# Optimization experiments

Hardware: AMD Instinct MI355X
Metric: run time of the kernel (lower is better)

Reference implementation:

```python
import jax, jax.numpy as jnp
import numpy as np

B, T, C, H = 128, 256, 512, 512

def setup_inputs() -> dict:
    key = jax.random.key(0)
    k1, k2, k3, k4 = jax.random.split(key, 4)
    x = jax.random.normal(k1, (B, T, C), dtype=jnp.float32)
    # nn.Linear(n_embed, H_size, bias=False).weight has shape [H, C]; scaled init
    s = 1.0 / np.sqrt(C)
    Wq = jax.random.normal(k2, (H, C), dtype=jnp.float32) * s
    Wk = jax.random.normal(k3, (H, C), dtype=jnp.float32) * s
    Wv = jax.random.normal(k4, (H, C), dtype=jnp.float32) * s
    return {"x": x, "Wq": Wq, "Wk": Wk, "Wv": Wv}

def reference(x, Wq, Wk, Wv):
    # q,k,v: [B,T,H] = x @ W.T (torch Linear convention)
    q = jnp.einsum('btc,hc->bth', x, Wq)
    k = jnp.einsum('btc,hc->bth', x, Wk)
    v = jnp.einsum('btc,hc->bth', x, Wv)
    scale = k.shape[-1] ** -0.5
    score = jnp.einsum('bqh,bkh->bqk', q, k) * scale  # [B,T,T]
    # causal mask: position j attends to i only if i <= j
    i = jnp.arange(T)
    causal = i[None, :] <= i[:, None]  # [T,T] lower-triangular
    score = jnp.where(causal[None, :, :], score, -jnp.inf)
    attn = jax.nn.softmax(score, axis=-1)
    # dropout is identity in eval mode
    out = jnp.einsum('bqk,bkh->bqh', attn, v)  # [B,T,H]
    return out
```

## Files before the change

### kernel.cpp

```cpp
#include <hip/hip_runtime.h>

#define B_ 128
#define T_ 256
#define C_ 512
#define H_ 512
#define CSCALE 0.063763824f

typedef _Float16 f16x8 __attribute__((ext_vector_type(8)));
typedef _Float16 f16x4 __attribute__((ext_vector_type(4)));
typedef float    f32x4 __attribute__((ext_vector_type(4)));

__device__ __forceinline__ void gld16(const void* gsrc, void* ldst) {
  __builtin_amdgcn_global_load_lds(
      (__attribute__((address_space(1))) void*)gsrc,
      (__attribute__((address_space(3))) void*)ldst, 16, 0, 0);
}

__global__ __launch_bounds__(256) void cvt_kernel(
    const float4* __restrict__ x, const float4* __restrict__ wq,
    const float4* __restrict__ wk, const float4* __restrict__ wv,
    f16x4* __restrict__ dst) {
  const int NX = (B_ * T_ * C_) / 4;
  const int NW = (H_ * C_) / 4;
  const int total = NX + 3 * NW;
  int gid = blockIdx.x * 256 + threadIdx.x;
  int gsz = gridDim.x * 256;
  for (int i = gid; i < total; i += gsz) {
    float4 f;
    if (i < NX)            f = x[i];
    else if (i < NX + NW)  f = wq[i - NX];
    else if (i < NX + 2*NW) f = wk[i - NX - NW];
    else                   f = wv[i - NX - 2*NW];
    f16x4 u = {(_Float16)f.x, (_Float16)f.y, (_Float16)f.z, (_Float16)f.w};
    dst[i] = u;
  }
}

__global__ __launch_bounds__(256) void proj_kernel(
    const _Float16* __restrict__ xh, const _Float16* __restrict__ wh,
    _Float16* __restrict__ qh, _Float16* __restrict__ kh,
    _Float16* __restrict__ vth) {
  __shared__ _Float16 As[128 * 32];
  __shared__ _Float16 Bs[128 * 32];

  const int tid  = threadIdx.x;
  const int lane = tid & 63;
  const int wave = tid >> 6;
  const int lr = lane & 15, lk = lane >> 4;
  const int m0 = blockIdx.x * 128;
  const int n0 = blockIdx.y * 128;
  const int z  = blockIdx.z;
  const _Float16* wz = wh + z * (H_ * C_);

  const int wm = (wave >> 1) * 64;
  const int wn = (wave & 1) * 64;

  f32x4 acc[4][4];
#pragma unroll
  for (int i = 0; i < 4; ++i)
#pragma unroll
    for (int j = 0; j < 4; ++j) acc[i][j] = {0.f, 0.f, 0.f, 0.f};

  const int srow = tid >> 2, scol = (tid & 3) * 8;
  const _Float16* aSrc = xh + (m0 + srow) * C_ + scol;
  const _Float16* bSrc = wz + (n0 + srow) * C_ + scol;

  for (int k0 = 0; k0 < C_; k0 += 32) {
    __syncthreads();
#pragma unroll
    for (int i = 0; i < 2; ++i) {
      gld16((const void*)(aSrc + i * 64 * C_ + k0), (void*)&As[i * 2048 + wave * 512]);
      gld16((const void*)(bSrc + i * 64 * C_ + k0), (void*)&Bs[i * 2048 + wave * 512]);
    }
    __syncthreads();

    f16x8 a[4], b[4];
#pragma unroll
    for (int mi = 0; mi < 4; ++mi)
      a[mi] = *(const f16x8*)&As[(wm + mi * 16 + lr) * 32 + lk * 8];
#pragma unroll
    for (int ni = 0; ni < 4; ++ni)
      b[ni] = *(const f16x8*)&Bs[(wn + ni * 16 + lr) * 32 + lk * 8];
#pragma unroll
    for (int mi = 0; mi < 4; ++mi)
#pragma unroll
      for (int ni = 0; ni < 4; ++ni)
        acc[mi][ni] = __builtin_amdgcn_mfma_f32_16x16x32_f16(a[mi], b[ni], acc[mi][ni], 0, 0, 0);
  }

  if (z < 2) {
    _Float16* out = (z == 0) ? qh : kh;
#pragma unroll
    for (int mi = 0; mi < 4; ++mi) {
      int mbase = m0 + wm + mi * 16 + lk * 4;
#pragma unroll
      for (int ni = 0; ni < 4; ++ni) {
        int n = n0 + wn + ni * 16 + lr;
#pragma unroll
        for (int r = 0; r < 4; ++r)
          out[(mbase + r) * H_ + n] = (_Float16)acc[mi][ni][r];
      }
    }
  } else {
#pragma unroll
    for (int mi = 0; mi < 4; ++mi) {
      int mbase = m0 + wm + mi * 16 + lk * 4;
      int bb = mbase >> 8, tt = mbase & 255;
#pragma unroll
      for (int ni = 0; ni < 4; ++ni) {
        int n = n0 + wn + ni * 16 + lr;
        f16x4 u = {(_Float16)acc[mi][ni][0], (_Float16)acc[mi][ni][1],
                   (_Float16)acc[mi][ni][2], (_Float16)acc[mi][ni][3]};
        *(f16x4*)&vth[bb * (H_ * T_) + n * T_ + tt] = u;
      }
    }
  }
}

__global__ __launch_bounds__(128) void attn_kernel(
    const _Float16* __restrict__ qh, const _Float16* __restrict__ kh,
    const _Float16* __restrict__ vth, float* __restrict__ dout) {
  __shared__ _Float16 Ps[2 * 16 * 40];

  const int tid  = threadIdx.x;
  const int lane = tid & 63;
  const int wq   = tid >> 6;
  const int lr = lane & 15, lk = lane >> 4;
  const int flat = blockIdx.x;
  const int xcd  = flat & 7;
  const int rest = flat >> 3;
  const int p    = rest & 7;
  const int g    = rest >> 3;
  const int b    = xcd + (g << 3);
  const int qw = wq ? (15 - p) : p;
  const int q0 = qw * 16;
  const int nkv = (qw >> 1) + 1;

  f16x8 qf[16];
  const _Float16* qrow = qh + ((size_t)b * T_ + q0 + lr) * H_;
#pragma unroll
  for (int f = 0; f < 16; ++f) qf[f] = *(const f16x8*)&qrow[f * 32 + lk * 8];

  f32x4 o[32];
#pragma unroll
  for (int i = 0; i < 32; ++i) o[i] = {0.f, 0.f, 0.f, 0.f};
  float m[4], l[4];
#pragma unroll
  for (int r = 0; r < 4; ++r) { m[r] = -1e30f; l[r] = 0.f; }

  const _Float16* kbase = kh + (size_t)b * T_ * H_;
  const _Float16* vbase = vth + (size_t)b * H_ * T_;
  _Float16* Pw = &Ps[wq * 640];

  for (int kvt = 0; kvt < nkv; ++kvt) {
    const int kv0 = kvt * 32;

    f32x4 s0 = {0.f, 0.f, 0.f, 0.f}, s1 = {0.f, 0.f, 0.f, 0.f};
    f32x4 t0 = {0.f, 0.f, 0.f, 0.f}, t1 = {0.f, 0.f, 0.f, 0.f};
    const _Float16* krow0 = kbase + (size_t)(kv0 + lr) * H_ + lk * 8;
    const _Float16* krow1 = krow0 + 16 * H_;
#pragma unroll
    for (int ks = 0; ks < 16; ks += 2) {
      f16x8 b0 = *(const f16x8*)&krow0[ks * 32];
      f16x8 b1 = *(const f16x8*)&krow1[ks * 32];
      f16x8 c0 = *(const f16x8*)&krow0[ks * 32 + 32];
      f16x8 c1 = *(const f16x8*)&krow1[ks * 32 + 32];
      s0 = __builtin_amdgcn_mfma_f32_16x16x32_f16(qf[ks], b0, s0, 0, 0, 0);
      s1 = __builtin_amdgcn_mfma_f32_16x16x32_f16(qf[ks], b1, s1, 0, 0, 0);
      t0 = __builtin_amdgcn_mfma_f32_16x16x32_f16(qf[ks + 1], c0, t0, 0, 0, 0);
      t1 = __builtin_amdgcn_mfma_f32_16x16x32_f16(qf[ks + 1], c1, t1, 0, 0, 0);
    }
    s0 = s0 + t0;
    s1 = s1 + t1;

    float p0[4], p1[4], rm[4];
    const int rowb = q0 + lk * 4;
#pragma unroll
    for (int r = 0; r < 4; ++r) {
      float v0 = (kv0 + lr      > rowb + r) ? -1e30f : s0[r];
      float v1 = (kv0 + 16 + lr > rowb + r) ? -1e30f : s1[r];
      s0[r] = v0; s1[r] = v1;
      rm[r] = fmaxf(v0, v1);
    }
#pragma unroll
    for (int off = 1; off < 16; off <<= 1)
#pragma unroll
      for (int r = 0; r < 4; ++r) rm[r] = fmaxf(rm[r], __shfl_xor(rm[r], off, 64));

    bool need = false;
#pragma unroll
    for (int r = 0; r < 4; ++r) need = need || (rm[r] > m[r] + 64.f);
    if (__any(need)) {
#pragma unroll
      for (int r = 0; r < 4; ++r) {
        float mn = fmaxf(m[r], rm[r]);
        float al = __builtin_amdgcn_exp2f((m[r] - mn) * CSCALE);
        m[r] = mn; l[r] *= al;
#pragma unroll
        for (int hf = 0; hf < 32; ++hf) o[hf][r] *= al;
      }
    }

    float rs[4];
#pragma unroll
    for (int r = 0; r < 4; ++r) {
      p0[r] = __builtin_amdgcn_exp2f((s0[r] - m[r]) * CSCALE);
      p1[r] = __builtin_amdgcn_exp2f((s1[r] - m[r]) * CSCALE);
      rs[r] = p0[r] + p1[r];
    }
#pragma unroll
    for (int off = 1; off < 16; off <<= 1)
#pragma unroll
      for (int r = 0; r < 4; ++r) rs[r] += __shfl_xor(rs[r], off, 64);
#pragma unroll
    for (int r = 0; r < 4; ++r) l[r] += rs[r];

#pragma unroll
    for (int r = 0; r < 4; ++r) {
      Pw[(lk * 4 + r) * 40 + lr]      = (_Float16)p0[r];
      Pw[(lk * 4 + r) * 40 + 16 + lr] = (_Float16)p1[r];
    }
    f16x8 pa = *(const f16x8*)&Pw[lr * 40 + lk * 8];

    const _Float16* vcol = vbase + (size_t)lr * T_ + kv0 + lk * 8;
#pragma unroll
    for (int hf = 0; hf < 32; ++hf) {
      f16x8 vb = *(const f16x8*)&vcol[(size_t)hf * 16 * T_];
      o[hf] = __builtin_amdgcn_mfma_f32_16x16x32_f16(pa, vb, o[hf], 0, 0, 0);
    }
  }

  float linv[4];
#pragma unroll
  for (int r = 0; r < 4; ++r) linv[r] = 1.0f / l[r];
  float* orow = dout + ((size_t)b * T_ + q0 + lk * 4) * H_;
#pragma unroll
  for (int hf = 0; hf < 32; ++hf)
#pragma unroll
    for (int r = 0; r < 4; ++r)
      orow[(size_t)r * H_ + hf * 16 + lr] = o[hf][r] * linv[r];
}

extern "C" void kernel_launch(void* const* d_in, const int* in_sizes, int n_in,
                              void* d_out, int out_size, void* d_ws, size_t ws_size,
                              hipStream_t stream) {
  const size_t NXE = (size_t)B_ * T_ * C_;
  const size_t NWE = (size_t)3 * H_ * C_;
  const size_t NQE = (size_t)B_ * T_ * H_;
  const size_t need = (NXE + NWE + 3 * NQE) * sizeof(_Float16);
  if (ws_size < need) return;

  const float* x  = (const float*)d_in[0];
  const float* wq = (const float*)d_in[1];
  const float* wk = (const float*)d_in[2];
  const float* wv = (const float*)d_in[3];

  _Float16* xh  = (_Float16*)d_ws;
  _Float16* wh  = xh + NXE;
  _Float16* qh  = wh + NWE;
  _Float16* kh  = qh + NQE;
  _Float16* vth = kh + NQE;

  cvt_kernel<<<2048, 256, 0, stream>>>((const float4*)x, (const float4*)wq,
                                       (const float4*)wk, (const float4*)wv,
                                       (f16x4*)xh);
  proj_kernel<<<dim3(256, 4, 3), dim3(256), 0, stream>>>(xh, wh, qh, kh, vth);
  attn_kernel<<<1024, 128, 0, stream>>>(qh, kh, vth, (float*)d_out);
}
```

Measured before the change: 202.2 us.

## Split attention head dimension across four waves with LDS score reduction

Each attention block now handles a single 16-row query tile, and its four waves each own a 128-wide slice of the head dimension. Every wave computes partial QK^T scores for its slice, and the partials are summed through shared memory with two barriers per KV tile. Per-thread registers for Q fragments and O accumulators drop to a quarter of what they were, which allows higher occupancy and twice as many blocks. In exchange, the softmax and exp work is duplicated across the four waves and the per-tile barriers add synchronisation cost.

```diff
diff --git a/kernel.cpp b/kernel.cpp
--- a/kernel.cpp
+++ b/kernel.cpp
@@ -117,10 +117,11 @@
   }
 }
 
-__global__ __launch_bounds__(128) void attn_kernel(
+__global__ __launch_bounds__(256, 4) void attn_kernel(
     const _Float16* __restrict__ qh, const _Float16* __restrict__ kh,
     const _Float16* __restrict__ vth, float* __restrict__ dout) {
-  __shared__ _Float16 Ps[2 * 16 * 40];
+  __shared__ f32x4 Sx[2][4][64];
+  __shared__ _Float16 Ps[4 * 16 * 40];
 
   const int tid  = threadIdx.x;
   const int lane = tid & 63;
@@ -129,49 +130,55 @@
   const int flat = blockIdx.x;
   const int xcd  = flat & 7;
   const int rest = flat >> 3;
-  const int p    = rest & 7;
-  const int g    = rest >> 3;
+  const int qw   = 15 - (rest & 15);
+  const int g    = rest >> 4;
   const int b    = xcd + (g << 3);
-  const int qw = wq ? (15 - p) : p;
   const int q0 = qw * 16;
   const int nkv = (qw >> 1) + 1;
-
-  f16x8 qf[16];
-  const _Float16* qrow = qh + ((size_t)b * T_ + q0 + lr) * H_;
-#pragma unroll
-  for (int f = 0; f < 16; ++f) qf[f] = *(const f16x8*)&qrow[f * 32 + lk * 8];
-
-  f32x4 o[32];
-#pragma unroll
-  for (int i = 0; i < 32; ++i) o[i] = {0.f, 0.f, 0.f, 0.f};
+  const int hbase = wq * 128;
+
+  f16x8 qf[4];
+  const _Float16* qrow = qh + ((size_t)b * T_ + q0 + lr) * H_ + hbase;
+#pragma unroll
+  for (int f = 0; f < 4; ++f) qf[f] = *(const f16x8*)&qrow[f * 32 + lk * 8];
+
+  f32x4 o[8];
+#pragma unroll
+  for (int i = 0; i < 8; ++i) o[i] = {0.f, 0.f, 0.f, 0.f};
   float m[4], l[4];
 #pragma unroll
   for (int r = 0; r < 4; ++r) { m[r] = -1e30f; l[r] = 0.f; }
 
-  const _Float16* kbase = kh + (size_t)b * T_ * H_;
-  const _Float16* vbase = vth + (size_t)b * H_ * T_;
+  const _Float16* kbase = kh + (size_t)b * T_ * H_ + hbase;
+  const _Float16* vbase = vth + ((size_t)b * H_ + hbase) * T_;
   _Float16* Pw = &Ps[wq * 640];
 
   for (int kvt = 0; kvt < nkv; ++kvt) {
     const int kv0 = kvt * 32;
 
     f32x4 s0 = {0.f, 0.f, 0.f, 0.f}, s1 = {0.f, 0.f, 0.f, 0.f};
-    f32x4 t0 = {0.f, 0.f, 0.f, 0.f}, t1 = {0.f, 0.f, 0.f, 0.f};
     const _Float16* krow0 = kbase + (size_t)(kv0 + lr) * H_ + lk * 8;
     const _Float16* krow1 = krow0 + 16 * H_;
 #pragma unroll
-    for (int ks = 0; ks < 16; ks += 2) {
+    for (int ks = 0; ks < 4; ++ks) {
       f16x8 b0 = *(const f16x8*)&krow0[ks * 32];
       f16x8 b1 = *(const f16x8*)&krow1[ks * 32];
-      f16x8 c0 = *(const f16x8*)&krow0[ks * 32 + 32];
-      f16x8 c1 = *(const f16x8*)&krow1[ks * 32 + 32];
       s0 = __builtin_amdgcn_mfma_f32_16x16x32_f16(qf[ks], b0, s0, 0, 0, 0);
       s1 = __builtin_amdgcn_mfma_f32_16x16x32_f16(qf[ks], b1, s1, 0, 0, 0);
-      t0 = __builtin_amdgcn_mfma_f32_16x16x32_f16(qf[ks + 1], c0, t0, 0, 0, 0);
-      t1 = __builtin_amdgcn_mfma_f32_16x16x32_f16(qf[ks + 1], c1, t1, 0, 0, 0);
-    }
-    s0 = s0 + t0;
-    s1 = s1 + t1;
+    }
+
+    Sx[0][wq][lane] = s0;
+    Sx[1][wq][lane] = s1;
+    __syncthreads();
+    {
+      f32x4 a0 = Sx[0][0][lane], a1 = Sx[0][1][lane];
+      f32x4 a2 = Sx[0][2][lane], a3 = Sx[0][3][lane];
+      s0 = (a0 + a1) + (a2 + a3);
+      f32x4 c0 = Sx[1][0][lane], c1 = Sx[1][1][lane];
+      f32x4 c2 = Sx[1][2][lane], c3 = Sx[1][3][lane];
+      s1 = (c0 + c1) + (c2 + c3);
+    }
+    __syncthreads();
 
     float p0[4], p1[4], rm[4];
     const int rowb = q0 + lk * 4;
@@ -197,7 +204,7 @@
         float al = __builtin_amdgcn_exp2f((m[r] - mn) * CSCALE);
         m[r] = mn; l[r] *= al;
 #pragma unroll
-        for (int hf = 0; hf < 32; ++hf) o[hf][r] *= al;
+        for (int hf = 0; hf < 8; ++hf) o[hf][r] *= al;
       }
     }
 
@@ -224,7 +231,7 @@
 
     const _Float16* vcol = vbase + (size_t)lr * T_ + kv0 + lk * 8;
 #pragma unroll
-    for (int hf = 0; hf < 32; ++hf) {
+    for (int hf = 0; hf < 8; ++hf) {
       f16x8 vb = *(const f16x8*)&vcol[(size_t)hf * 16 * T_];
       o[hf] = __builtin_amdgcn_mfma_f32_16x16x32_f16(pa, vb, o[hf], 0, 0, 0);
     }
@@ -233,9 +240,9 @@
   float linv[4];
 #pragma unroll
   for (int r = 0; r < 4; ++r) linv[r] = 1.0f / l[r];
-  float* orow = dout + ((size_t)b * T_ + q0 + lk * 4) * H_;
-#pragma unroll
-  for (int hf = 0; hf < 32; ++hf)
+  float* orow = dout + ((size_t)b * T_ + q0 + lk * 4) * H_ + hbase;
+#pragma unroll
+  for (int hf = 0; hf < 8; ++hf)
 #pragma unroll
     for (int r = 0; r < 4; ++r)
       orow[(size_t)r * H_ + hf * 16 + lr] = o[hf][r] * linv[r];
@@ -265,5 +272,5 @@
                                        (const float4*)wk, (const float4*)wv,
                                        (f16x4*)xh);
   proj_kernel<<<dim3(256, 4, 3), dim3(256), 0, stream>>>(xh, wh, qh, kh, vth);
-  attn_kernel<<<1024, 128, 0, stream>>>(qh, kh, vth, (float*)d_out);
-}
+  attn_kernel<<<2048, 256, 0, stream>>>(qh, kh, vth, (float*)d_out);
+}
```

Measured after the change: 199.4 us. Within noise of the previous version (-1.4%).

## Split attention head dimension across four waves with 32x32 MFMA and LDS score reduction

Applied to the files above, without the earlier changes.

Rewrites the attention kernel so each 256-thread block handles one 32-row query tile. The four waves each own a 128-wide slice of the head dimension, compute partial QK^T scores with 32x32x16 MFMAs, and sum those partial scores through a double-buffered LDS exchange behind a block barrier. P is rebuilt in registers using lane shuffles rather than an LDS round trip, and outputs are written as float4 vectors. The goal is to cut per-wave register pressure (accumulators shrink from 32 f32x4 to 4 f32x16) and raise occupancy. The cost is a __syncthreads per KV tile, redundant softmax work in every wave, and load imbalance now spread across whole blocks instead of being paired within a block.

```diff
diff --git a/kernel.cpp b/kernel.cpp
--- a/kernel.cpp
+++ b/kernel.cpp
@@ -8,7 +8,11 @@
 
 typedef _Float16 f16x8 __attribute__((ext_vector_type(8)));
 typedef _Float16 f16x4 __attribute__((ext_vector_type(4)));
+typedef _Float16 f16x2 __attribute__((ext_vector_type(2)));
 typedef float    f32x4 __attribute__((ext_vector_type(4)));
+typedef float    f32x16 __attribute__((ext_vector_type(16)));
+typedef unsigned int u32;
+typedef u32 u32x4 __attribute__((ext_vector_type(4)));
 
 __device__ __forceinline__ void gld16(const void* gsrc, void* ldst) {
   __builtin_amdgcn_global_load_lds(
@@ -117,128 +121,133 @@
   }
 }
 
-__global__ __launch_bounds__(128) void attn_kernel(
+__global__ __launch_bounds__(256, 2) void attn_kernel(
     const _Float16* __restrict__ qh, const _Float16* __restrict__ kh,
     const _Float16* __restrict__ vth, float* __restrict__ dout) {
-  __shared__ _Float16 Ps[2 * 16 * 40];
+  __shared__ f32x4 Ex[2][4][4][64];
 
   const int tid  = threadIdx.x;
   const int lane = tid & 63;
   const int wq   = tid >> 6;
-  const int lr = lane & 15, lk = lane >> 4;
+  const int lq   = lane & 31;
+  const int hi   = lane >> 5;
   const int flat = blockIdx.x;
   const int xcd  = flat & 7;
   const int rest = flat >> 3;
-  const int p    = rest & 7;
+  const int qb   = 7 - (rest & 7);
   const int g    = rest >> 3;
   const int b    = xcd + (g << 3);
-  const int qw = wq ? (15 - p) : p;
-  const int q0 = qw * 16;
-  const int nkv = (qw >> 1) + 1;
-
-  f16x8 qf[16];
-  const _Float16* qrow = qh + ((size_t)b * T_ + q0 + lr) * H_;
-#pragma unroll
-  for (int f = 0; f < 16; ++f) qf[f] = *(const f16x8*)&qrow[f * 32 + lk * 8];
-
-  f32x4 o[32];
-#pragma unroll
-  for (int i = 0; i < 32; ++i) o[i] = {0.f, 0.f, 0.f, 0.f};
-  float m[4], l[4];
-#pragma unroll
-  for (int r = 0; r < 4; ++r) { m[r] = -1e30f; l[r] = 0.f; }
-
-  const _Float16* kbase = kh + (size_t)b * T_ * H_;
-  const _Float16* vbase = vth + (size_t)b * H_ * T_;
-  _Float16* Pw = &Ps[wq * 640];
+  const int q0   = qb * 32;
+  const int nkv  = qb + 1;
+  const int hbase = wq * 128;
+  const int qg   = q0 + lq;
+
+  f16x8 qf[8];
+  const _Float16* qp = qh + ((size_t)b * T_ + qg) * H_ + hbase + hi * 8;
+#pragma unroll
+  for (int ks = 0; ks < 8; ++ks) qf[ks] = *(const f16x8*)&qp[ks * 16];
+
+  f32x16 ot[4];
+#pragma unroll
+  for (int i = 0; i < 4; ++i) ot[i] = {};
+  float m_ = -1e30f, l_ = 0.f;
+
+  const _Float16* kp = kh  + ((size_t)b * T_ + lq) * H_ + hbase + hi * 8;
+  const _Float16* vp = vth + ((size_t)b * H_ + hbase + lq) * T_ + hi * 8;
 
   for (int kvt = 0; kvt < nkv; ++kvt) {
     const int kv0 = kvt * 32;
 
-    f32x4 s0 = {0.f, 0.f, 0.f, 0.f}, s1 = {0.f, 0.f, 0.f, 0.f};
-    f32x4 t0 = {0.f, 0.f, 0.f, 0.f}, t1 = {0.f, 0.f, 0.f, 0.f};
-    const _Float16* krow0 = kbase + (size_t)(kv0 + lr) * H_ + lk * 8;
-    const _Float16* krow1 = krow0 + 16 * H_;
-#pragma unroll
-    for (int ks = 0; ks < 16; ks += 2) {
-      f16x8 b0 = *(const f16x8*)&krow0[ks * 32];
-      f16x8 b1 = *(const f16x8*)&krow1[ks * 32];
-      f16x8 c0 = *(const f16x8*)&krow0[ks * 32 + 32];
-      f16x8 c1 = *(const f16x8*)&krow1[ks * 32 + 32];
-      s0 = __builtin_amdgcn_mfma_f32_16x16x32_f16(qf[ks], b0, s0, 0, 0, 0);
-      s1 = __builtin_amdgcn_mfma_f32_16x16x32_f16(qf[ks], b1, s1, 0, 0, 0);
-      t0 = __builtin_amdgcn_mfma_f32_16x16x32_f16(qf[ks + 1], c0, t0, 0, 0, 0);
-      t1 = __builtin_amdgcn_mfma_f32_16x16x32_f16(qf[ks + 1], c1, t1, 0, 0, 0);
-    }
-    s0 = s0 + t0;
-    s1 = s1 + t1;
-
-    float p0[4], p1[4], rm[4];
-    const int rowb = q0 + lk * 4;
-#pragma unroll
-    for (int r = 0; r < 4; ++r) {
-      float v0 = (kv0 + lr      > rowb + r) ? -1e30f : s0[r];
-      float v1 = (kv0 + 16 + lr > rowb + r) ? -1e30f : s1[r];
-      s0[r] = v0; s1[r] = v1;
-      rm[r] = fmaxf(v0, v1);
-    }
-#pragma unroll
-    for (int off = 1; off < 16; off <<= 1)
-#pragma unroll
-      for (int r = 0; r < 4; ++r) rm[r] = fmaxf(rm[r], __shfl_xor(rm[r], off, 64));
-
-    bool need = false;
-#pragma unroll
-    for (int r = 0; r < 4; ++r) need = need || (rm[r] > m[r] + 64.f);
-    if (__any(need)) {
-#pragma unroll
-      for (int r = 0; r < 4; ++r) {
-        float mn = fmaxf(m[r], rm[r]);
-        float al = __builtin_amdgcn_exp2f((m[r] - mn) * CSCALE);
-        m[r] = mn; l[r] *= al;
-#pragma unroll
-        for (int hf = 0; hf < 32; ++hf) o[hf][r] *= al;
+    f16x8 kf[8];
+#pragma unroll
+    for (int ks = 0; ks < 8; ++ks)
+      kf[ks] = *(const f16x8*)&kp[(size_t)kv0 * H_ + ks * 16];
+    f32x16 st = {};
+#pragma unroll
+    for (int ks = 0; ks < 8; ++ks)
+      st = __builtin_amdgcn_mfma_f32_32x32x16_f16(kf[ks], qf[ks], st, 0, 0, 0);
+
+    const int buf = kvt & 1;
+#pragma unroll
+    for (int c = 0; c < 4; ++c) {
+      f32x4 w4 = {st[c*4+0], st[c*4+1], st[c*4+2], st[c*4+3]};
+      Ex[buf][wq][c][lane] = w4;
+    }
+    __syncthreads();
+#pragma unroll
+    for (int ow = 0; ow < 4; ++ow) {
+      if (ow == wq) continue;
+#pragma unroll
+      for (int c = 0; c < 4; ++c) {
+        f32x4 r4 = Ex[buf][ow][c][lane];
+        st[c*4+0] += r4[0]; st[c*4+1] += r4[1];
+        st[c*4+2] += r4[2]; st[c*4+3] += r4[3];
       }
     }
 
-    float rs[4];
-#pragma unroll
-    for (int r = 0; r < 4; ++r) {
-      p0[r] = __builtin_amdgcn_exp2f((s0[r] - m[r]) * CSCALE);
-      p1[r] = __builtin_amdgcn_exp2f((s1[r] - m[r]) * CSCALE);
-      rs[r] = p0[r] + p1[r];
-    }
-#pragma unroll
-    for (int off = 1; off < 16; off <<= 1)
-#pragma unroll
-      for (int r = 0; r < 4; ++r) rs[r] += __shfl_xor(rs[r], off, 64);
-#pragma unroll
-    for (int r = 0; r < 4; ++r) l[r] += rs[r];
-
-#pragma unroll
-    for (int r = 0; r < 4; ++r) {
-      Pw[(lk * 4 + r) * 40 + lr]      = (_Float16)p0[r];
-      Pw[(lk * 4 + r) * 40 + 16 + lr] = (_Float16)p1[r];
-    }
-    f16x8 pa = *(const f16x8*)&Pw[lr * 40 + lk * 8];
-
-    const _Float16* vcol = vbase + (size_t)lr * T_ + kv0 + lk * 8;
-#pragma unroll
-    for (int hf = 0; hf < 32; ++hf) {
-      f16x8 vb = *(const f16x8*)&vcol[(size_t)hf * 16 * T_];
-      o[hf] = __builtin_amdgcn_mfma_f32_16x16x32_f16(pa, vb, o[hf], 0, 0, 0);
-    }
-  }
-
-  float linv[4];
-#pragma unroll
-  for (int r = 0; r < 4; ++r) linv[r] = 1.0f / l[r];
-  float* orow = dout + ((size_t)b * T_ + q0 + lk * 4) * H_;
-#pragma unroll
-  for (int hf = 0; hf < 32; ++hf)
-#pragma unroll
-    for (int r = 0; r < 4; ++r)
-      orow[(size_t)r * H_ + hf * 16 + lr] = o[hf][r] * linv[r];
+    float p[16], rm = -1e30f;
+    const int kvb = kv0 + 4 * hi;
+#pragma unroll
+    for (int r = 0; r < 16; ++r) {
+      int kvg = kvb + (r & 3) + 8 * (r >> 2);
+      float v = (kvg > qg) ? -1e30f : st[r];
+      p[r] = v;
+      rm = fmaxf(rm, v);
+    }
+    rm = fmaxf(rm, __shfl_xor(rm, 32, 64));
+
+    if (__any((int)(rm > m_ + 64.f))) {
+      float mn = fmaxf(m_, rm);
+      float al = __builtin_amdgcn_exp2f((m_ - mn) * CSCALE);
+      m_ = mn; l_ *= al;
+#pragma unroll
+      for (int i = 0; i < 4; ++i)
+#pragma unroll
+        for (int e = 0; e < 16; ++e) ot[i][e] *= al;
+    }
+    float rs = 0.f;
+#pragma unroll
+    for (int r = 0; r < 16; ++r) {
+      p[r] = __builtin_amdgcn_exp2f((p[r] - m_) * CSCALE);
+      rs += p[r];
+    }
+    rs += __shfl_xor(rs, 32, 64);
+    l_ += rs;
+
+    u32 w[8], sw[8];
+#pragma unroll
+    for (int i = 0; i < 8; ++i) {
+      f16x2 h2; h2[0] = (_Float16)p[2*i]; h2[1] = (_Float16)p[2*i+1];
+      w[i] = __builtin_bit_cast(u32, h2);
+    }
+#pragma unroll
+    for (int i = 0; i < 8; ++i) sw[i] = (u32)__shfl_xor((int)w[i], 32, 64);
+    u32x4 t0 = { hi ? sw[2] : w[0],  hi ? sw[3] : w[1],
+                 hi ? w[2]  : sw[0], hi ? w[3]  : sw[1] };
+    u32x4 t1 = { hi ? sw[6] : w[4],  hi ? sw[7] : w[5],
+                 hi ? w[6]  : sw[4], hi ? w[7]  : sw[5] };
+    f16x8 pb0 = __builtin_bit_cast(f16x8, t0);
+    f16x8 pb1 = __builtin_bit_cast(f16x8, t1);
+
+#pragma unroll
+    for (int ht = 0; ht < 4; ++ht) {
+      f16x8 va0 = *(const f16x8*)&vp[(size_t)(ht * 32) * T_ + kv0];
+      f16x8 va1 = *(const f16x8*)&vp[(size_t)(ht * 32) * T_ + kv0 + 16];
+      ot[ht] = __builtin_amdgcn_mfma_f32_32x32x16_f16(va0, pb0, ot[ht], 0, 0, 0);
+      ot[ht] = __builtin_amdgcn_mfma_f32_32x32x16_f16(va1, pb1, ot[ht], 0, 0, 0);
+    }
+  }
+
+  float li = 1.0f / l_;
+  float* op = dout + ((size_t)b * T_ + qg) * H_ + hbase + 4 * hi;
+#pragma unroll
+  for (int ht = 0; ht < 4; ++ht)
+#pragma unroll
+    for (int rq = 0; rq < 4; ++rq) {
+      f32x4 v4 = {ot[ht][rq*4+0] * li, ot[ht][rq*4+1] * li,
+                  ot[ht][rq*4+2] * li, ot[ht][rq*4+3] * li};
+      *(f32x4*)&op[ht * 32 + rq * 8] = v4;
+    }
 }
 
 extern "C" void kernel_launch(void* const* d_in, const int* in_sizes, int n_in,
@@ -265,5 +274,5 @@
                                        (const float4*)wk, (const float4*)wv,
                                        (f16x4*)xh);
   proj_kernel<<<dim3(256, 4, 3), dim3(256), 0, stream>>>(xh, wh, qh, kh, vth);
-  attn_kernel<<<1024, 128, 0, stream>>>(qh, kh, vth, (float*)d_out);
-}
+  attn_kernel<<<1024, 256, 0, stream>>>(qh, kh, vth, (float*)d_out);
+}
```

Result: faster. 175.7 us (-13.1%).
